# Performance work log

Measured on AMD Instinct MI355X. Metric: run time of the kernel, lower is better.

The kernel has to match this reference:

```python
import jax, jax.numpy as jnp
import numpy as np

CHANNEL = 1
ALPHA = 1.0
EPS = 1e-10
SHAPE = (1, CHANNEL, 160, 192, 160)


def _sobel_kernels(channel):
    s2 = np.array([[-1., 0., 1.], [-2., 0., 2.], [-1., 0., 1.]], dtype=np.float32)
    # sobel.repeat(channel,1,3,1,1): 2D kernel tiled along depth -> k[d,h,w] = s2[h,w]
    kx = np.tile(s2[None, :, :], (3, 1, 1))
    ky = np.tile(s2.T[None, :, :], (3, 1, 1))
    kz = np.array([[[-1., -1., -1.], [-2., -2., -2.], [-1., -1., -1.]],
                   [[0., 0., 0.], [0., 0., 0.], [0., 0., 0.]],
                   [[1., 1., 1.], [2., 2., 2.], [1., 1., 1.]]], dtype=np.float32)
    def rep(k):  # -> [channel, 1, 3, 3, 3] for depthwise conv
        return jnp.asarray(np.tile(k[None, None], (channel, 1, 1, 1, 1)))
    return rep(kx), rep(ky), rep(kz)


def _conv3d(x, k, channel):
    # torch F.conv3d (cross-correlation), padding=1, groups=channel
    return jax.lax.conv_general_dilated(
        x, k, window_strides=(1, 1, 1), padding=((1, 1), (1, 1), (1, 1)),
        dimension_numbers=('NCDHW', 'OIDHW', 'NCDHW'),
        feature_group_count=channel)


def setup_inputs() -> dict:
    key = jax.random.key(0)
    k1, k2, k3 = jax.random.split(key, 3)
    M = jax.random.normal(k1, SHAPE, dtype=jnp.float32)
    S = jax.random.normal(k2, SHAPE, dtype=jnp.float32)
    flow = jax.random.normal(k3, (SHAPE[0], 3) + SHAPE[2:], dtype=jnp.float32)
    return {"M": M, "S": S, "flow": flow}


def reference(M, S, flow):
    kx, ky, kz = _sobel_kernels(CHANNEL)
    Idiff = M - S
    Sx = _conv3d(S, kx, CHANNEL)
    Sy = _conv3d(S, ky, CHANNEL)
    Sz = _conv3d(S, kz, CHANNEL)
    Mx = _conv3d(M, kx, CHANNEL)
    My = _conv3d(M, ky, CHANNEL)
    Mz = _conv3d(M, kz, CHANNEL)
    Sxyz_mag = Sx ** 2 + Sy ** 2 + Sz ** 2
    Mxyz_mag = Mx ** 2 + My ** 2 + Mz ** 2
    denom_S = Sxyz_mag + (ALPHA ** 2) * Idiff ** 2 + 1e-10
    denom_M = Mxyz_mag + (ALPHA ** 2) * Idiff ** 2 + 1e-10
    Ux = Idiff * (Sx / denom_S + Mx / denom_M)
    Uy = Idiff * (Sy / denom_S + My / denom_M)
    Uz = Idiff * (Sz / denom_S + Mz / denom_M)
    demons_ori_xz = jnp.arctan(Ux / (Uz + EPS))
    demons_ori_yz = jnp.arctan(Uy / (Uz + EPS))
    flow_ori_xz = jnp.arctan(flow[:, 0] / (flow[:, 2] + EPS))
    flow_ori_yz = jnp.arctan(flow[:, 1] / (flow[:, 2] + EPS))
    ori_error = jnp.mean((flow_ori_xz - demons_ori_xz) ** 2) + \
                jnp.mean((flow_ori_yz - demons_ori_yz) ** 2)
    return ori_error
```

## Files before the change

kernel.cpp:

```cpp
#include <hip/hip_runtime.h>
#include <math.h>

#define DD 160
#define HH 192
#define WW 160
#define TW 32
#define TH 8
#define TD 16
#define HW (HH * WW)
#define NVOX (DD * HH * WW)
#define HTW (TW + 2)
#define HTH (TH + 2)
#define HALO (HTW * HTH)

__device__ __forceinline__ int mod3(int x) { return ((x % 3) + 3) % 3; }

__global__ __launch_bounds__(256) void demons_ori_kernel(
    const float* __restrict__ Mv, const float* __restrict__ Sv,
    const float* __restrict__ flow, float* __restrict__ out)
{
    __shared__ float raw[2][3][HTH][HTW];
    __shared__ float Aa[2][HTH][HTW];
    __shared__ float Dz[2][HTH][HTW];
    __shared__ float redbuf[4];

    const int tid = threadIdx.x;
    const int tw = tid & 31;
    const int th = tid >> 5;

    const int w0 = blockIdx.x * TW;
    const int h0 = blockIdx.y * TH;
    const int d0 = blockIdx.z * TD;

    auto load_slice = [&](int d, int slot) {
        const bool din = (d >= 0) && (d < DD);
        for (int i = tid; i < HALO; i += 256) {
            int hh = i / HTW;
            int ww = i - hh * HTW;
            int gh = h0 + hh - 1;
            int gw = w0 + ww - 1;
            float vs = 0.f, vm = 0.f;
            if (din && gh >= 0 && gh < HH && gw >= 0 && gw < WW) {
                size_t off = (size_t)d * HW + (size_t)gh * WW + gw;
                vs = Sv[off];
                vm = Mv[off];
            }
            raw[0][slot][hh][ww] = vs;
            raw[1][slot][hh][ww] = vm;
        }
    };

    load_slice(d0 - 1, mod3(d0 - 1));
    load_slice(d0,     mod3(d0));

    float lsum = 0.f;

    for (int dd = 0; dd < TD; ++dd) {
        const int d = d0 + dd;
        const int sm = mod3(d - 1), s0 = mod3(d), sp = mod3(d + 1);

        load_slice(d + 1, sp);
        __syncthreads();

        for (int i = tid; i < HALO; i += 256) {
            int hh = i / HTW;
            int ww = i - hh * HTW;
            float xm0 = raw[0][sm][hh][ww];
            float x00 = raw[0][s0][hh][ww];
            float xp0 = raw[0][sp][hh][ww];
            Aa[0][hh][ww] = xm0 + x00 + xp0;
            Dz[0][hh][ww] = xp0 - xm0;
            float xm1 = raw[1][sm][hh][ww];
            float x01 = raw[1][s0][hh][ww];
            float xp1 = raw[1][sp][hh][ww];
            Aa[1][hh][ww] = xm1 + x01 + xp1;
            Dz[1][hh][ww] = xp1 - xm1;
        }
        __syncthreads();

        const int hc = th + 1, wc = tw + 1;
        float gx[2], gy[2], gz[2];
        #pragma unroll
        for (int f = 0; f < 2; ++f) {
            float a_mm = Aa[f][hc - 1][wc - 1];
            float a_m0 = Aa[f][hc - 1][wc];
            float a_mp = Aa[f][hc - 1][wc + 1];
            float a_0m = Aa[f][hc][wc - 1];
            float a_0p = Aa[f][hc][wc + 1];
            float a_pm = Aa[f][hc + 1][wc - 1];
            float a_p0 = Aa[f][hc + 1][wc];
            float a_pp = Aa[f][hc + 1][wc + 1];
            gx[f] = (a_mp + 2.f * a_0p + a_pp) - (a_mm + 2.f * a_0m + a_pm);
            gy[f] = (a_pm + 2.f * a_p0 + a_pp) - (a_mm + 2.f * a_m0 + a_mp);
            float d_mm = Dz[f][hc - 1][wc - 1];
            float d_m0 = Dz[f][hc - 1][wc];
            float d_mp = Dz[f][hc - 1][wc + 1];
            float d_0m = Dz[f][hc][wc - 1];
            float d_00 = Dz[f][hc][wc];
            float d_0p = Dz[f][hc][wc + 1];
            float d_pm = Dz[f][hc + 1][wc - 1];
            float d_p0 = Dz[f][hc + 1][wc];
            float d_pp = Dz[f][hc + 1][wc + 1];
            gz[f] = (d_mm + d_m0 + d_mp) + 2.f * (d_0m + d_00 + d_0p)
                  + (d_pm + d_p0 + d_pp);
        }

        float sc = raw[0][s0][hc][wc];
        float mc = raw[1][s0][hc][wc];
        float idf = mc - sc;
        float i2 = idf * idf;
        float denS = gx[0] * gx[0] + gy[0] * gy[0] + gz[0] * gz[0] + i2 + 1e-10f;
        float denM = gx[1] * gx[1] + gy[1] * gy[1] + gz[1] * gz[1] + i2 + 1e-10f;
        float rS = 1.f / denS;
        float rM = 1.f / denM;
        float Ux = idf * (gx[0] * rS + gx[1] * rM);
        float Uy = idf * (gy[0] * rS + gy[1] * rM);
        float Uz = idf * (gz[0] * rS + gz[1] * rM);
        float rz = 1.f / (Uz + 1e-10f);
        float dxz = atanf(Ux * rz);
        float dyz = atanf(Uy * rz);

        size_t off = (size_t)d * HW + (size_t)(h0 + th) * WW + (w0 + tw);
        float f0 = flow[off];
        float f1 = flow[(size_t)NVOX + off];
        float f2 = flow[2 * (size_t)NVOX + off];
        float rf = 1.f / (f2 + 1e-10f);
        float fxz = atanf(f0 * rf);
        float fyz = atanf(f1 * rf);

        float e1 = fxz - dxz;
        float e2 = fyz - dyz;
        lsum += e1 * e1 + e2 * e2;
    }

    #pragma unroll
    for (int o = 32; o > 0; o >>= 1)
        lsum += __shfl_down(lsum, o, 64);
    if ((tid & 63) == 0)
        redbuf[tid >> 6] = lsum;
    __syncthreads();
    if (tid == 0) {
        float s = redbuf[0] + redbuf[1] + redbuf[2] + redbuf[3];
        atomicAdd(out, s * (1.0f / (float)NVOX));
    }
}

extern "C" void kernel_launch(void* const* d_in, const int* in_sizes, int n_in,
                              void* d_out, int out_size, void* d_ws, size_t ws_size,
                              hipStream_t stream) {
    const float* Mv   = (const float*)d_in[0];
    const float* Sv   = (const float*)d_in[1];
    const float* flow = (const float*)d_in[2];
    float* out = (float*)d_out;

    hipMemsetAsync(out, 0, sizeof(float), stream);

    dim3 grid(WW / TW, HH / TH, DD / TD);
    demons_ori_kernel<<<grid, dim3(256), 0, stream>>>(Mv, Sv, flow, out);
}
```

Measured before the change: 156.5 us.

## Separate Sobel into per-slice 2D partials, use fast atan and rcp

Each depth slice is now reduced to per-thread 2D Sobel partials (x, y and smoothing terms) held in registers and rolled across slices, replacing the three-slice shared ring and the Aa/Dz intermediate pass. Shared memory drops to a double buffer with one barrier per slice, and halo address setup is precomputed. The depth tile is halved to TD=8, doubling the block count. Exact divisions and atanf are swapped for hardware reciprocal and a polynomial atan, which cuts ALU work but lowers accuracy.

```diff
diff --git a/kernel.cpp b/kernel.cpp
--- a/kernel.cpp
+++ b/kernel.cpp
@@ -6,131 +6,138 @@
 #define WW 160
 #define TW 32
 #define TH 8
-#define TD 16
+#define TD 8
 #define HW (HH * WW)
 #define NVOX (DD * HH * WW)
 #define HTW (TW + 2)
 #define HTH (TH + 2)
 #define HALO (HTW * HTH)
 
-__device__ __forceinline__ int mod3(int x) { return ((x % 3) + 3) % 3; }
+__device__ __forceinline__ float atan_fast(float r) {
+    float ar = fabsf(r);
+    float inv = __builtin_amdgcn_rcpf(ar);
+    bool big = ar > 1.0f;
+    float x = big ? inv : ar;
+    float x2 = x * x;
+    float p = fmaf(x2, fmaf(x2, fmaf(x2, fmaf(x2, fmaf(x2,
+              -0.0117212f, 0.05265332f), -0.11643287f), 0.19354346f),
+              -0.33262347f), 0.99997726f);
+    p *= x;
+    float res = big ? (1.57079632679489662f - p) : p;
+    return copysignf(res, r);
+}
 
 __global__ __launch_bounds__(256) void demons_ori_kernel(
     const float* __restrict__ Mv, const float* __restrict__ Sv,
     const float* __restrict__ flow, float* __restrict__ out)
 {
-    __shared__ float raw[2][3][HTH][HTW];
-    __shared__ float Aa[2][HTH][HTW];
-    __shared__ float Dz[2][HTH][HTW];
+    __shared__ float buf[2][2][HTH][HTW];
     __shared__ float redbuf[4];
 
     const int tid = threadIdx.x;
     const int tw = tid & 31;
     const int th = tid >> 5;
-
     const int w0 = blockIdx.x * TW;
     const int h0 = blockIdx.y * TH;
     const int d0 = blockIdx.z * TD;
 
-    auto load_slice = [&](int d, int slot) {
+    int nst = 0;
+    int sidx[2];
+    int gbase[2];
+    bool gok[2];
+    for (int i = tid; i < HALO; i += 256) {
+        int hh = i / HTW, ww = i - hh * HTW;
+        int gh = h0 + hh - 1, gw = w0 + ww - 1;
+        sidx[nst] = i;
+        gok[nst] = (gh >= 0 && gh < HH && gw >= 0 && gw < WW);
+        gbase[nst] = gh * WW + gw;
+        nst++;
+    }
+
+    const int hc = th + 1, wc = tw + 1;
+
+    auto stage = [&](int d, float pq[2][4]) {
+        float* __restrict__ bS = &buf[d & 1][0][0][0];
+        float* __restrict__ bM = &buf[d & 1][1][0][0];
         const bool din = (d >= 0) && (d < DD);
-        for (int i = tid; i < HALO; i += 256) {
-            int hh = i / HTW;
-            int ww = i - hh * HTW;
-            int gh = h0 + hh - 1;
-            int gw = w0 + ww - 1;
+        for (int j = 0; j < nst; ++j) {
             float vs = 0.f, vm = 0.f;
-            if (din && gh >= 0 && gh < HH && gw >= 0 && gw < WW) {
-                size_t off = (size_t)d * HW + (size_t)gh * WW + gw;
+            if (din && gok[j]) {
+                size_t off = (size_t)d * HW + gbase[j];
                 vs = Sv[off];
                 vm = Mv[off];
             }
-            raw[0][slot][hh][ww] = vs;
-            raw[1][slot][hh][ww] = vm;
+            bS[sidx[j]] = vs;
+            bM[sidx[j]] = vm;
+        }
+        __syncthreads();
+        #pragma unroll
+        for (int f = 0; f < 2; ++f) {
+            const float* __restrict__ b = f ? bM : bS;
+            const float* r0 = b + (hc - 1) * HTW + (wc - 1);
+            const float* r1 = r0 + HTW;
+            const float* r2 = r1 + HTW;
+            float v00 = r0[0], v01 = r0[1], v02 = r0[2];
+            float v10 = r1[0], v11 = r1[1], v12 = r1[2];
+            float v20 = r2[0], v21 = r2[1], v22 = r2[2];
+            pq[f][0] = (v02 + 2.f * v12 + v22) - (v00 + 2.f * v10 + v20);
+            pq[f][1] = (v20 + 2.f * v21 + v22) - (v00 + 2.f * v01 + v02);
+            pq[f][2] = (v00 + v01 + v02) + 2.f * (v10 + v11 + v12)
+                     + (v20 + v21 + v22);
+            pq[f][3] = v11;
         }
     };
 
-    load_slice(d0 - 1, mod3(d0 - 1));
-    load_slice(d0,     mod3(d0));
+    float Pm[2][4], P0[2][4], Pp[2][4];
+    stage(d0 - 1, Pm);
+    stage(d0, P0);
 
     float lsum = 0.f;
+    const size_t voff0 = (size_t)(h0 + th) * WW + (w0 + tw);
 
+    #pragma unroll
     for (int dd = 0; dd < TD; ++dd) {
         const int d = d0 + dd;
-        const int sm = mod3(d - 1), s0 = mod3(d), sp = mod3(d + 1);
+        stage(d + 1, Pp);
 
-        load_slice(d + 1, sp);
-        __syncthreads();
+        float idf = P0[1][3] - P0[0][3];
+        float i2 = idf * idf + 1e-10f;
+        float gxS = Pm[0][0] + P0[0][0] + Pp[0][0];
+        float gyS = Pm[0][1] + P0[0][1] + Pp[0][1];
+        float gzS = Pp[0][2] - Pm[0][2];
+        float gxM = Pm[1][0] + P0[1][0] + Pp[1][0];
+        float gyM = Pm[1][1] + P0[1][1] + Pp[1][1];
+        float gzM = Pp[1][2] - Pm[1][2];
+        float denS = gxS * gxS + gyS * gyS + gzS * gzS + i2;
+        float denM = gxM * gxM + gyM * gyM + gzM * gzM + i2;
+        float rS = __builtin_amdgcn_rcpf(denS);
+        float rM = __builtin_amdgcn_rcpf(denM);
+        float Ux = idf * (gxS * rS + gxM * rM);
+        float Uy = idf * (gyS * rS + gyM * rM);
+        float Uz = idf * (gzS * rS + gzM * rM);
+        float rz = __builtin_amdgcn_rcpf(Uz + 1e-10f);
+        float dxz = atan_fast(Ux * rz);
+        float dyz = atan_fast(Uy * rz);
 
-        for (int i = tid; i < HALO; i += 256) {
-            int hh = i / HTW;
-            int ww = i - hh * HTW;
-            float xm0 = raw[0][sm][hh][ww];
-            float x00 = raw[0][s0][hh][ww];
-            float xp0 = raw[0][sp][hh][ww];
-            Aa[0][hh][ww] = xm0 + x00 + xp0;
-            Dz[0][hh][ww] = xp0 - xm0;
-            float xm1 = raw[1][sm][hh][ww];
-            float x01 = raw[1][s0][hh][ww];
-            float xp1 = raw[1][sp][hh][ww];
-            Aa[1][hh][ww] = xm1 + x01 + xp1;
-            Dz[1][hh][ww] = xp1 - xm1;
-        }
-        __syncthreads();
-
-        const int hc = th + 1, wc = tw + 1;
-        float gx[2], gy[2], gz[2];
-        #pragma unroll
-        for (int f = 0; f < 2; ++f) {
-            float a_mm = Aa[f][hc - 1][wc - 1];
-            float a_m0 = Aa[f][hc - 1][wc];
-            float a_mp = Aa[f][hc - 1][wc + 1];
-            float a_0m = Aa[f][hc][wc - 1];
-            float a_0p = Aa[f][hc][wc + 1];
-            float a_pm = Aa[f][hc + 1][wc - 1];
-            float a_p0 = Aa[f][hc + 1][wc];
-            float a_pp = Aa[f][hc + 1][wc + 1];
-            gx[f] = (a_mp + 2.f * a_0p + a_pp) - (a_mm + 2.f * a_0m + a_pm);
-            gy[f] = (a_pm + 2.f * a_p0 + a_pp) - (a_mm + 2.f * a_m0 + a_mp);
-            float d_mm = Dz[f][hc - 1][wc - 1];
-            float d_m0 = Dz[f][hc - 1][wc];
-            float d_mp = Dz[f][hc - 1][wc + 1];
-            float d_0m = Dz[f][hc][wc - 1];
-            float d_00 = Dz[f][hc][wc];
-            float d_0p = Dz[f][hc][wc + 1];
-            float d_pm = Dz[f][hc + 1][wc - 1];
-            float d_p0 = Dz[f][hc + 1][wc];
-            float d_pp = Dz[f][hc + 1][wc + 1];
-            gz[f] = (d_mm + d_m0 + d_mp) + 2.f * (d_0m + d_00 + d_0p)
-                  + (d_pm + d_p0 + d_pp);
-        }
-
-        float sc = raw[0][s0][hc][wc];
-        float mc = raw[1][s0][hc][wc];
-        float idf = mc - sc;
-        float i2 = idf * idf;
-        float denS = gx[0] * gx[0] + gy[0] * gy[0] + gz[0] * gz[0] + i2 + 1e-10f;
-        float denM = gx[1] * gx[1] + gy[1] * gy[1] + gz[1] * gz[1] + i2 + 1e-10f;
-        float rS = 1.f / denS;
-        float rM = 1.f / denM;
-        float Ux = idf * (gx[0] * rS + gx[1] * rM);
-        float Uy = idf * (gy[0] * rS + gy[1] * rM);
-        float Uz = idf * (gz[0] * rS + gz[1] * rM);
-        float rz = 1.f / (Uz + 1e-10f);
-        float dxz = atanf(Ux * rz);
-        float dyz = atanf(Uy * rz);
-
-        size_t off = (size_t)d * HW + (size_t)(h0 + th) * WW + (w0 + tw);
+        size_t off = (size_t)d * HW + voff0;
         float f0 = flow[off];
         float f1 = flow[(size_t)NVOX + off];
         float f2 = flow[2 * (size_t)NVOX + off];
-        float rf = 1.f / (f2 + 1e-10f);
-        float fxz = atanf(f0 * rf);
-        float fyz = atanf(f1 * rf);
+        float rf = __builtin_amdgcn_rcpf(f2 + 1e-10f);
+        float fxz = atan_fast(f0 * rf);
+        float fyz = atan_fast(f1 * rf);
 
         float e1 = fxz - dxz;
         float e2 = fyz - dyz;
         lsum += e1 * e1 + e2 * e2;
+
+        #pragma unroll
+        for (int f = 0; f < 2; ++f)
+            #pragma unroll
+            for (int q = 0; q < 4; ++q) {
+                Pm[f][q] = P0[f][q];
+                P0[f][q] = Pp[f][q];
+            }
     }
 
     #pragma unroll
```

Result: faster. 153.2 us (-2.1%).
